# Optimization experiments

Measured on AMD Instinct MI355X. Metric: run time of the kernel, lower is better.

Reference implementation:

```python
import jax, jax.numpy as jnp
import numpy as np

N_NODES = 50000
KEEP_PROB = 0.5  # dropout = 0.5


def setup_inputs() -> dict:
    key = jax.random.key(0)
    k1, k2, k3, k4, k5 = jax.random.split(key, 5)
    S, E, DIN, DOUT = 2, 800000, 512, 128
    x = jax.random.normal(k1, (N_NODES, DIN), dtype=jnp.float32)
    weights = jax.random.normal(k2, (S, DIN, DOUT), dtype=jnp.float32) * (1.0 / np.sqrt(DIN))
    adj_rows = jax.random.randint(k3, (S, E), 0, N_NODES, dtype=jnp.int32)
    adj_cols = jax.random.randint(k4, (S, E), 0, N_NODES, dtype=jnp.int32)
    adj_vals = jax.random.uniform(k5, (S, E), dtype=jnp.float32)
    return {"x": x, "weights": weights, "adj_rows": adj_rows,
            "adj_cols": adj_cols, "adj_vals": adj_vals}


def reference(x, weights, adj_rows, adj_cols, adj_vals):
    # Dropout (TF semantics: mask and scale by 1/keep_prob), fixed key for determinism.
    mask = (jax.random.uniform(jax.random.key(42), x.shape) < KEEP_PROB)
    xd = x * mask.astype(x.dtype) / KEEP_PROB
    # Dense GEMM per support: pre_sup[s] = dropout(x) @ W_s  -> [S, N, Dout]
    pre_sup = jnp.einsum('nd,sdo->sno', xd, weights)
    # SpMM per support: out[s] = A_s @ pre_sup[s] with A_s in COO form.
    def spmm(rows, cols, vals, h):
        return jax.ops.segment_sum(vals[:, None] * h[cols], rows,
                                   num_segments=N_NODES)
    out = jax.vmap(spmm)(adj_rows, adj_cols, adj_vals, pre_sup)  # [S, N, Dout]
    return jax.nn.relu(out)
```

## Files before the change

### kernel.cpp

```cpp
#include <hip/hip_runtime.h>
#include <stdint.h>

#define N_NODES 50000
#define DIN     512
#define DOUT    128
#define NSUP    2
#define EDGES   800000
#define NEDGE   (NSUP * EDGES)
#define NROWS   (NSUP * N_NODES)
#define NB      782
#define CH      8192
#define NCH     ((NEDGE + CH - 1) / CH)
#define EPT     16
#define SCAP    4096

typedef __attribute__((ext_vector_type(8))) short short8;
typedef __attribute__((ext_vector_type(4))) float f32x4;

__device__ __forceinline__ uint32_t rotl32(uint32_t v, uint32_t d) {
  return (v << d) | (v >> (32u - d));
}

__device__ __forceinline__ void threefry2x32(uint32_t x0, uint32_t x1,
                                             uint32_t& o0, uint32_t& o1) {
  const uint32_t ks0 = 0u;
  const uint32_t ks1 = 42u;
  const uint32_t ks2 = 0u ^ 42u ^ 0x1BD11BDAu;
  x0 += ks0; x1 += ks1;
#define TF_R(r) { x0 += x1; x1 = rotl32(x1, (r)); x1 ^= x0; }
  TF_R(13) TF_R(15) TF_R(26) TF_R(6)
  x0 += ks1; x1 += ks2 + 1u;
  TF_R(17) TF_R(29) TF_R(16) TF_R(24)
  x0 += ks2; x1 += ks0 + 2u;
  TF_R(13) TF_R(15) TF_R(26) TF_R(6)
  x0 += ks0; x1 += ks1 + 3u;
  TF_R(17) TF_R(29) TF_R(16) TF_R(24)
  x0 += ks1; x1 += ks2 + 4u;
  TF_R(13) TF_R(15) TF_R(26) TF_R(6)
  x0 += ks2; x1 += ks0 + 5u;
#undef TF_R
  o0 = x0; o1 = x1;
}

__device__ __forceinline__ bool keep_mask(uint32_t idx) {
  uint32_t o0, o1;
  threefry2x32(0u, idx, o0, o1);
  uint32_t bits = o0 ^ o1;
  float u = __uint_as_float((bits >> 9) | 0x3F800000u) - 1.0f;
  return u < 0.5f;
}

__device__ __forceinline__ uint32_t pack_bf16x2(float a, float b) {
  uint32_t ua = __float_as_uint(a), ub = __float_as_uint(b);
  ua += 0x7fffu + ((ua >> 16) & 1u);
  ub += 0x7fffu + ((ub >> 16) & 1u);
  return (ua >> 16) | (ub & 0xffff0000u);
}

__device__ __forceinline__ uint32_t bf16rne(float f) {
  uint32_t u = __float_as_uint(f);
  u += 0x7fffu + ((u >> 16) & 1u);
  return u >> 16;
}

__global__ __launch_bounds__(256) void wcvt(const float* __restrict__ w,
                                            unsigned short* __restrict__ b16t) {
  int i = blockIdx.x * 256 + threadIdx.x;
  if (i >= NSUP * DIN * DOUT) return;
  int s   = i >> 16;
  int rem = i & 65535;
  int k   = rem >> 7;
  int o   = rem & 127;
  b16t[(size_t)(s * DOUT + o) * DIN + k] = (unsigned short)bf16rne(w[i]);
}

__global__ __launch_bounds__(512) void gemm_mfma(
    const float* __restrict__ x, const unsigned short* __restrict__ b16t,
    unsigned short* __restrict__ pre16) {
  __shared__ unsigned short As[64 * 64];
  __shared__ unsigned short Bs[256 * 64];
  const int t    = threadIdx.x;
  const int lane = t & 63;
  const int w    = t >> 6;
  const int wr   = w >> 2;
  const int wc   = w & 3;
  const int m0   = blockIdx.x * 64;

  f32x4 acc[2][4];
#pragma unroll
  for (int i = 0; i < 2; ++i)
#pragma unroll
    for (int j = 0; j < 4; ++j) acc[i][j] = (f32x4){0.f, 0.f, 0.f, 0.f};

  const int arow  = t >> 3;
  const int ak8   = (t & 7) * 8;
  const int agrow = m0 + arow;
  const int aswz  = (arow * 64 + ak8) ^ ((arow & 7) << 3);

  for (int kc = 0; kc < DIN; kc += 64) {
    __syncthreads();
    {
      union { uint32_t u[4]; short8 s; } pk;
      if (agrow < N_NODES) {
        const float4* src = reinterpret_cast<const float4*>(
            x + (size_t)agrow * DIN + kc + ak8);
        float4 v0 = src[0], v1 = src[1];
        float f[8] = {v0.x, v0.y, v0.z, v0.w, v1.x, v1.y, v1.z, v1.w};
        uint32_t base = (uint32_t)(agrow * DIN + kc + ak8);
#pragma unroll
        for (int q = 0; q < 8; ++q)
          f[q] = keep_mask(base + q) ? f[q] * 2.0f : 0.0f;
#pragma unroll
        for (int q = 0; q < 4; ++q) pk.u[q] = pack_bf16x2(f[2 * q], f[2 * q + 1]);
      } else {
#pragma unroll
        for (int q = 0; q < 4; ++q) pk.u[q] = 0u;
      }
      *reinterpret_cast<short8*>(&As[aswz]) = pk.s;
    }
#pragma unroll
    for (int i = 0; i < 4; ++i) {
      int c   = i * 512 + t;
      int col = c >> 3;
      int k8  = (c & 7) * 8;
      short8 v = *reinterpret_cast<const short8*>(
          b16t + (size_t)col * DIN + kc + k8);
      *reinterpret_cast<short8*>(&Bs[(col * 64 + k8) ^ ((col & 7) << 3)]) = v;
    }
    __syncthreads();

    short8 af[2][2], bf[2][4];
#pragma unroll
    for (int mf = 0; mf < 2; ++mf)
#pragma unroll
      for (int kk = 0; kk < 2; ++kk) {
        int row = wr * 32 + mf * 16 + (lane & 15);
        int idx = (row * 64 + kk * 32 + (lane >> 4) * 8) ^ ((row & 7) << 3);
        af[mf][kk] = *reinterpret_cast<const short8*>(&As[idx]);
      }
#pragma unroll
    for (int kk = 0; kk < 2; ++kk)
#pragma unroll
      for (int nf = 0; nf < 4; ++nf) {
        int col = wc * 64 + nf * 16 + (lane & 15);
        int idx = (col * 64 + kk * 32 + (lane >> 4) * 8) ^ ((col & 7) << 3);
        bf[kk][nf] = *reinterpret_cast<const short8*>(&Bs[idx]);
      }
#pragma unroll
    for (int mf = 0; mf < 2; ++mf)
#pragma unroll
      for (int nf = 0; nf < 4; ++nf)
#pragma unroll
        for (int kk = 0; kk < 2; ++kk)
          acc[mf][nf] = __builtin_amdgcn_mfma_f32_16x16x32_bf16(
              af[mf][kk], bf[kk][nf], acc[mf][nf], 0, 0, 0);
  }

#pragma unroll
  for (int mf = 0; mf < 2; ++mf) {
    int rbase = m0 + wr * 32 + mf * 16 + ((lane >> 4) * 4);
#pragma unroll
    for (int nf = 0; nf < 4; ++nf) {
      int col = wc * 64 + nf * 16 + (lane & 15);
      int s = col >> 7, o = col & 127;
#pragma unroll
      for (int q = 0; q < 4; ++q) {
        int row = rbase + q;
        if (row < N_NODES)
          pre16[(size_t)(s * N_NODES + row) * DOUT + o] =
              (unsigned short)bf16rne(acc[mf][nf][q]);
      }
    }
  }
}

__global__ __launch_bounds__(512) void count_b(const int* __restrict__ rows,
                                               int* __restrict__ gcnt) {
  __shared__ int hist[NB];
  int t = threadIdx.x;
  for (int b = t; b < NB; b += 512) hist[b] = 0;
  __syncthreads();
  int e0 = blockIdx.x * CH;
#pragma unroll
  for (int i = 0; i < EPT; ++i) {
    int e = e0 + i * 512 + t;
    if (e < NEDGE) {
      int s = (e >= EDGES) ? 1 : 0;
      int grow = s * N_NODES + rows[e];
      atomicAdd(&hist[grow >> 7], 1);
    }
  }
  __syncthreads();
  for (int b = t; b < NB; b += 512)
    if (hist[b]) atomicAdd(&gcnt[b], hist[b]);
}

__global__ __launch_bounds__(1024) void scan782(const int* __restrict__ gcnt,
                                                int* __restrict__ bstart,
                                                int* __restrict__ gcursor) {
  __shared__ int sm[1024];
  int t = threadIdx.x;
  int c = (t < NB) ? gcnt[t] : 0;
  sm[t] = c;
  __syncthreads();
  for (int d = 1; d < 1024; d <<= 1) {
    int v = sm[t];
    int a = (t >= d) ? sm[t - d] : 0;
    __syncthreads();
    sm[t] = v + a;
    __syncthreads();
  }
  if (t < NB) {
    int ex = sm[t] - c;
    bstart[t] = ex;
    gcursor[t] = ex;
  }
  if (t == NB - 1) bstart[NB] = sm[t];
}

__global__ __launch_bounds__(512) void bin_scatter(
    const int* __restrict__ rows, const int* __restrict__ cols,
    const float* __restrict__ vals, int* __restrict__ gcursor,
    uint64_t* __restrict__ binned) {
  __shared__ uint32_t hist[NB];
  __shared__ uint32_t hexcl[NB];
  __shared__ uint32_t sbase[NB];
  __shared__ uint32_t scanb[512];
  __shared__ uint64_t ordered[CH];
  __shared__ uint16_t bk16[CH];
  int t = threadIdx.x;
  for (int b = t; b < NB; b += 512) hist[b] = 0;
  __syncthreads();
  int e0 = blockIdx.x * CH;
  uint32_t key[EPT], rank[EPT], bkt[EPT], vbits[EPT];
#pragma unroll
  for (int i = 0; i < EPT; ++i) {
    int e = e0 + i * 512 + t;
    if (e < NEDGE) {
      int s = (e >= EDGES) ? 1 : 0;
      uint32_t grow = (uint32_t)(s * N_NODES + rows[e]);
      uint32_t gcol = (uint32_t)(s * N_NODES + cols[e]);
      vbits[i] = __float_as_uint(vals[e]);
      uint32_t b = grow >> 7;
      bkt[i] = b;
      key[i] = ((grow & 127u) << 17) | gcol;
      rank[i] = atomicAdd(&hist[b], 1u);
    } else {
      bkt[i] = 0xFFFFFFFFu;
    }
  }
  __syncthreads();
  int t2 = t * 2;
  uint32_t a0 = (t2 < NB) ? hist[t2] : 0u;
  uint32_t a1 = (t2 + 1 < NB) ? hist[t2 + 1] : 0u;
  scanb[t] = a0 + a1;
  __syncthreads();
  for (int d = 1; d < 512; d <<= 1) {
    uint32_t v = scanb[t];
    uint32_t a = (t >= d) ? scanb[t - d] : 0u;
    __syncthreads();
    scanb[t] = v + a;
    __syncthreads();
  }
  uint32_t base  = t ? scanb[t - 1] : 0u;
  uint32_t total = scanb[511];
  if (t2 < NB)     hexcl[t2]     = base;
  if (t2 + 1 < NB) hexcl[t2 + 1] = base + a0;
  for (int b = t; b < NB; b += 512)
    if (hist[b]) sbase[b] = (uint32_t)atomicAdd(&gcursor[b], (int)hist[b]);
  __syncthreads();
#pragma unroll
  for (int i = 0; i < EPT; ++i) {
    if (bkt[i] != 0xFFFFFFFFu) {
      uint32_t slot = hexcl[bkt[i]] + rank[i];
      ordered[slot] = ((uint64_t)vbits[i] << 32) | key[i];
      bk16[slot] = (uint16_t)bkt[i];
    }
  }
  __syncthreads();
#pragma unroll
  for (int i = 0; i < EPT; ++i) {
    uint32_t slot = (uint32_t)(i * 512 + t);
    if (slot < total) {
      uint32_t b = bk16[slot];
      uint32_t dst = sbase[b] + (slot - hexcl[b]);
      binned[dst] = ordered[slot];
    }
  }
}

__global__ __launch_bounds__(512) void sort_bucket(
    const int* __restrict__ bstart, uint64_t* __restrict__ binned,
    int* __restrict__ row_start) {
  __shared__ uint64_t ordered[SCAP];
  __shared__ uint32_t hist[128];
  __shared__ uint32_t excl[128];
  const int t = threadIdx.x;
  const int b = blockIdx.x;
  const int beg = bstart[b], end = bstart[b + 1];
  const int cnt = end - beg;
  if (t < 128) hist[t] = 0;
  __syncthreads();
  uint64_t ed[8];
  uint32_t rk[8], rw[8];
#pragma unroll
  for (int i = 0; i < 8; ++i) {
    int slot = i * 512 + t;
    if (slot < cnt) {
      uint64_t e = binned[beg + slot];
      ed[i] = e;
      uint32_t rowin = ((uint32_t)e >> 17) & 127u;
      rw[i] = rowin;
      rk[i] = atomicAdd(&hist[rowin], 1u);
    } else {
      rw[i] = 0xFFFFFFFFu;
    }
  }
  __syncthreads();
  if (t < 128) excl[t] = hist[t];
  __syncthreads();
  for (int d = 1; d < 128; d <<= 1) {
    uint32_t v = (t < 128) ? excl[t] : 0u;
    uint32_t a = (t >= d && t < 128) ? excl[t - d] : 0u;
    __syncthreads();
    if (t < 128) excl[t] = v + a;
    __syncthreads();
  }
  if (t < 128) {
    uint32_t ex = excl[t] - hist[t];
    int grow = b * 128 + t;
    if (grow < NROWS) row_start[grow] = beg + (int)ex;
    excl[t] = ex;
  }
  __syncthreads();
#pragma unroll
  for (int i = 0; i < 8; ++i)
    if (rw[i] != 0xFFFFFFFFu)
      ordered[excl[rw[i]] + rk[i]] = ed[i];
  __syncthreads();
#pragma unroll
  for (int i = 0; i < 8; ++i) {
    int slot = i * 512 + t;
    if (slot < cnt) binned[beg + slot] = ordered[slot];
  }
  if (b == 0 && t == 0) row_start[NROWS] = NEDGE;
}

__global__ __launch_bounds__(256) void spmm_pull(
    const int* __restrict__ row_start, const uint64_t* __restrict__ binned,
    const uint32_t* __restrict__ preu, float* __restrict__ out) {
  int rid  = blockIdx.x * 4 + (threadIdx.x >> 6);
  int lane = threadIdx.x & 63;
  if (rid >= NROWS) return;
  int beg = row_start[rid];
  int end = row_start[rid + 1];
  float a0 = 0.f, a1 = 0.f;
  int j = beg;
  for (; j + 4 <= end; j += 4) {
    uint64_t e0 = binned[j],     e1 = binned[j + 1];
    uint64_t e2 = binned[j + 2], e3 = binned[j + 3];
    uint32_t q0 = preu[(size_t)((uint32_t)e0 & 0x1FFFFu) * 64 + lane];
    uint32_t q1 = preu[(size_t)((uint32_t)e1 & 0x1FFFFu) * 64 + lane];
    uint32_t q2 = preu[(size_t)((uint32_t)e2 & 0x1FFFFu) * 64 + lane];
    uint32_t q3 = preu[(size_t)((uint32_t)e3 & 0x1FFFFu) * 64 + lane];
    float v0 = __uint_as_float((uint32_t)(e0 >> 32));
    float v1 = __uint_as_float((uint32_t)(e1 >> 32));
    float v2 = __uint_as_float((uint32_t)(e2 >> 32));
    float v3 = __uint_as_float((uint32_t)(e3 >> 32));
    a0 += v0 * __uint_as_float(q0 << 16);
    a1 += v0 * __uint_as_float(q0 & 0xffff0000u);
    a0 += v1 * __uint_as_float(q1 << 16);
    a1 += v1 * __uint_as_float(q1 & 0xffff0000u);
    a0 += v2 * __uint_as_float(q2 << 16);
    a1 += v2 * __uint_as_float(q2 & 0xffff0000u);
    a0 += v3 * __uint_as_float(q3 << 16);
    a1 += v3 * __uint_as_float(q3 & 0xffff0000u);
  }
  for (; j < end; ++j) {
    uint64_t e = binned[j];
    uint32_t q = preu[(size_t)((uint32_t)e & 0x1FFFFu) * 64 + lane];
    float v = __uint_as_float((uint32_t)(e >> 32));
    a0 += v * __uint_as_float(q << 16);
    a1 += v * __uint_as_float(q & 0xffff0000u);
  }
  float2 o = make_float2(fmaxf(a0, 0.f), fmaxf(a1, 0.f));
  *reinterpret_cast<float2*>(out + (size_t)rid * DOUT + 2 * lane) = o;
}

extern "C" void kernel_launch(void* const* d_in, const int* in_sizes, int n_in,
                              void* d_out, int out_size, void* d_ws, size_t ws_size,
                              hipStream_t stream) {
  const float* x    = (const float*)d_in[0];
  const float* w    = (const float*)d_in[1];
  const int*   rows = (const int*)d_in[2];
  const int*   cols = (const int*)d_in[3];
  const float* vals = (const float*)d_in[4];
  float* out = (float*)d_out;

  uint32_t* base = (uint32_t*)d_ws;
  uint32_t* preu = base;
  unsigned short* b16t = (unsigned short*)(base + 6400000);
  int* gcnt      = (int*)(base + 6400000 + 65536);
  int* bstart    = gcnt + 800;
  int* gcursor   = bstart + 800;
  int* row_start = gcursor + 800;
  uint64_t* binned = (uint64_t*)(row_start + 100004);
  size_t need = ((size_t)6400000 + 65536 + 2400 + 100004 + 3200000) * 4;
  if (ws_size < need) return;

  hipMemsetAsync(gcnt, 0, NB * sizeof(int), stream);

  wcvt<<<(NSUP * DIN * DOUT + 255) / 256, 256, 0, stream>>>(w, b16t);

  gemm_mfma<<<(N_NODES + 63) / 64, 512, 0, stream>>>(x, b16t,
                                                     (unsigned short*)preu);

  count_b<<<NCH, 512, 0, stream>>>(rows, gcnt);
  scan782<<<1, 1024, 0, stream>>>(gcnt, bstart, gcursor);
  bin_scatter<<<NCH, 512, 0, stream>>>(rows, cols, vals, gcursor, binned);
  sort_bucket<<<NB, 512, 0, stream>>>(bstart, binned, row_start);

  spmm_pull<<<(NROWS + 3) / 4, 256, 0, stream>>>(row_start, binned, preu, out);
}
```

Measured before the change: 218.4 us.

## Precompute dropout mask bitfield and enlarge GEMM M-tile to 128 rows

Adds a maskgen kernel that computes the threefry dropout mask once into a packed bit buffer, so the GEMM reads 8 mask bits per load instead of running threefry per element inside the A-tile staging. The GEMM tile grows from 64 to 128 rows per block, each wave doing 4x4 MFMA fragments, which reuses each staged B tile across more rows and halves the block count. In exchange it adds an extra launch and a 3.2 MB mask write/read, uses more registers and LDS per block, and leaves fewer blocks (391) to spread across the CUs.

```diff
diff --git a/kernel.cpp b/kernel.cpp
--- a/kernel.cpp
+++ b/kernel.cpp
@@ -13,6 +13,7 @@
 #define NCH     ((NEDGE + CH - 1) / CH)
 #define EPT     16
 #define SCAP    4096
+#define NMASKW  ((N_NODES * DIN) / 32)
 
 typedef __attribute__((ext_vector_type(8))) short short8;
 typedef __attribute__((ext_vector_type(4))) float f32x4;
@@ -63,6 +64,17 @@
   return u >> 16;
 }
 
+__global__ __launch_bounds__(256) void maskgen(uint32_t* __restrict__ maskbuf) {
+  int wid = blockIdx.x * 256 + threadIdx.x;
+  if (wid >= NMASKW) return;
+  uint32_t base = (uint32_t)wid * 32u;
+  uint32_t m = 0u;
+#pragma unroll 4
+  for (int q = 0; q < 32; ++q)
+    m |= (keep_mask(base + q) ? 1u : 0u) << q;
+  maskbuf[wid] = m;
+}
+
 __global__ __launch_bounds__(256) void wcvt(const float* __restrict__ w,
                                             unsigned short* __restrict__ b16t) {
   int i = blockIdx.x * 256 + threadIdx.x;
@@ -74,67 +86,68 @@
   b16t[(size_t)(s * DOUT + o) * DIN + k] = (unsigned short)bf16rne(w[i]);
 }
 
-__global__ __launch_bounds__(512) void gemm_mfma(
-    const float* __restrict__ x, const unsigned short* __restrict__ b16t,
+__global__ __launch_bounds__(512) void gemm_mfma2(
+    const float* __restrict__ x, const uint32_t* __restrict__ maskbuf,
+    const unsigned short* __restrict__ b16t,
     unsigned short* __restrict__ pre16) {
-  __shared__ unsigned short As[64 * 64];
+  __shared__ unsigned short As[128 * 64];
   __shared__ unsigned short Bs[256 * 64];
   const int t    = threadIdx.x;
   const int lane = t & 63;
   const int w    = t >> 6;
   const int wr   = w >> 2;
   const int wc   = w & 3;
-  const int m0   = blockIdx.x * 64;
-
-  f32x4 acc[2][4];
-#pragma unroll
-  for (int i = 0; i < 2; ++i)
+  const int m0   = blockIdx.x * 128;
+
+  f32x4 acc[4][4];
+#pragma unroll
+  for (int i = 0; i < 4; ++i)
 #pragma unroll
     for (int j = 0; j < 4; ++j) acc[i][j] = (f32x4){0.f, 0.f, 0.f, 0.f};
 
-  const int arow  = t >> 3;
-  const int ak8   = (t & 7) * 8;
-  const int agrow = m0 + arow;
-  const int aswz  = (arow * 64 + ak8) ^ ((arow & 7) << 3);
-
   for (int kc = 0; kc < DIN; kc += 64) {
     __syncthreads();
-    {
+#pragma unroll
+    for (int i = 0; i < 2; ++i) {
+      int slot = i * 512 + t;
+      int row  = slot >> 3;
+      int k8   = (slot & 7) * 8;
+      int grow = m0 + row;
       union { uint32_t u[4]; short8 s; } pk;
-      if (agrow < N_NODES) {
-        const float4* src = reinterpret_cast<const float4*>(
-            x + (size_t)agrow * DIN + kc + ak8);
+      if (grow < N_NODES) {
+        uint32_t b8 = (uint32_t)grow * DIN + (uint32_t)(kc + k8);
+        const float4* src = reinterpret_cast<const float4*>(x + b8);
         float4 v0 = src[0], v1 = src[1];
         float f[8] = {v0.x, v0.y, v0.z, v0.w, v1.x, v1.y, v1.z, v1.w};
-        uint32_t base = (uint32_t)(agrow * DIN + kc + ak8);
+        uint32_t bits = maskbuf[b8 >> 5] >> (b8 & 31u);
 #pragma unroll
         for (int q = 0; q < 8; ++q)
-          f[q] = keep_mask(base + q) ? f[q] * 2.0f : 0.0f;
+          f[q] = ((bits >> q) & 1u) ? f[q] * 2.0f : 0.0f;
 #pragma unroll
         for (int q = 0; q < 4; ++q) pk.u[q] = pack_bf16x2(f[2 * q], f[2 * q + 1]);
       } else {
 #pragma unroll
         for (int q = 0; q < 4; ++q) pk.u[q] = 0u;
       }
-      *reinterpret_cast<short8*>(&As[aswz]) = pk.s;
+      *reinterpret_cast<short8*>(&As[(row * 64 + k8) ^ ((row & 7) << 3)]) = pk.s;
     }
 #pragma unroll
     for (int i = 0; i < 4; ++i) {
-      int c   = i * 512 + t;
-      int col = c >> 3;
-      int k8  = (c & 7) * 8;
+      int slot = i * 512 + t;
+      int col  = slot >> 3;
+      int k8   = (slot & 7) * 8;
       short8 v = *reinterpret_cast<const short8*>(
           b16t + (size_t)col * DIN + kc + k8);
       *reinterpret_cast<short8*>(&Bs[(col * 64 + k8) ^ ((col & 7) << 3)]) = v;
     }
     __syncthreads();
 
-    short8 af[2][2], bf[2][4];
-#pragma unroll
-    for (int mf = 0; mf < 2; ++mf)
+    short8 af[4][2], bf[2][4];
+#pragma unroll
+    for (int mf = 0; mf < 4; ++mf)
 #pragma unroll
       for (int kk = 0; kk < 2; ++kk) {
-        int row = wr * 32 + mf * 16 + (lane & 15);
+        int row = wr * 64 + mf * 16 + (lane & 15);
         int idx = (row * 64 + kk * 32 + (lane >> 4) * 8) ^ ((row & 7) << 3);
         af[mf][kk] = *reinterpret_cast<const short8*>(&As[idx]);
       }
@@ -147,7 +160,7 @@
         bf[kk][nf] = *reinterpret_cast<const short8*>(&Bs[idx]);
       }
 #pragma unroll
-    for (int mf = 0; mf < 2; ++mf)
+    for (int mf = 0; mf < 4; ++mf)
 #pragma unroll
       for (int nf = 0; nf < 4; ++nf)
 #pragma unroll
@@ -157,8 +170,8 @@
   }
 
 #pragma unroll
-  for (int mf = 0; mf < 2; ++mf) {
-    int rbase = m0 + wr * 32 + mf * 16 + ((lane >> 4) * 4);
+  for (int mf = 0; mf < 4; ++mf) {
+    int rbase = m0 + wr * 64 + mf * 16 + ((lane >> 4) * 4);
 #pragma unroll
     for (int nf = 0; nf < 4; ++nf) {
       int col = wc * 64 + nf * 16 + (lane & 15);
@@ -398,22 +411,24 @@
   float* out = (float*)d_out;
 
   uint32_t* base = (uint32_t*)d_ws;
-  uint32_t* preu = base;
+  uint32_t* preu       = base;
   unsigned short* b16t = (unsigned short*)(base + 6400000);
-  int* gcnt      = (int*)(base + 6400000 + 65536);
+  uint32_t* maskbuf    = base + 6400000 + 65536;
+  int* gcnt      = (int*)(base + 6400000 + 65536 + 800000);
   int* bstart    = gcnt + 800;
   int* gcursor   = bstart + 800;
   int* row_start = gcursor + 800;
   uint64_t* binned = (uint64_t*)(row_start + 100004);
-  size_t need = ((size_t)6400000 + 65536 + 2400 + 100004 + 3200000) * 4;
+  size_t need = ((size_t)6400000 + 65536 + 800000 + 2400 + 100004 + 3200000) * 4;
   if (ws_size < need) return;
 
   hipMemsetAsync(gcnt, 0, NB * sizeof(int), stream);
 
+  maskgen<<<(NMASKW + 255) / 256, 256, 0, stream>>>(maskbuf);
   wcvt<<<(NSUP * DIN * DOUT + 255) / 256, 256, 0, stream>>>(w, b16t);
 
-  gemm_mfma<<<(N_NODES + 63) / 64, 512, 0, stream>>>(x, b16t,
-                                                     (unsigned short*)preu);
+  gemm_mfma2<<<(N_NODES + 127) / 128, 512, 0, stream>>>(x, maskbuf, b16t,
+                                                        (unsigned short*)preu);
 
   count_b<<<NCH, 512, 0, stream>>>(rows, gcnt);
   scan782<<<1, 1024, 0, stream>>>(gcnt, bstart, gcursor);
```

After: 216.8 us. Within noise of the previous version (-0.7%).
